# Kernel optimization log

Hardware: AMD Instinct MI355X
Metric: run time of the kernel (lower is better)

The kernel has to match this reference:

```python
import jax, jax.numpy as jnp
import numpy as np

B, DIM, T = 8, 1024, 2048      # batch, hidden_size, frames
CD, K, Q = 128, 1024, 8        # codebook_dim, codebook_size, num_quantizers


def setup_inputs() -> dict:
    key = jax.random.key(0)
    ks = jax.random.split(key, 5)
    return {
        "embeddings": jax.random.normal(ks[0], (B, DIM, T), jnp.float32),
        # stacked per-quantizer params (scan axis = Q)
        "W_in": jax.random.normal(ks[1], (Q, DIM, CD), jnp.float32) * 0.02,
        "b_in": jnp.zeros((Q, CD), jnp.float32),
        "W_out": jax.random.normal(ks[2], (Q, CD, DIM), jnp.float32) * 0.02,
        "b_out": jnp.zeros((Q, DIM), jnp.float32),
        "embed": jax.random.normal(ks[3], (Q, K, CD), jnp.float32),
    }


def _rvq_forward(embeddings, W_in, b_in, W_out, b_out, embed):
    """Residual VQ: sequentially quantize residual with Q euclidean codebooks.
    Returns (quantized_sum [B,DIM,T], codes [Q,B,T])."""

    def step(carry, params):
        residual, acc = carry
        Wi, bi, Wo, bo, E = params
        # project_in after permute(0,2,1): [B,T,CD]
        h = jnp.einsum('bdt,dc->btc', residual, Wi) + bi
        # squared euclidean distance to codebook entries: [B,T,K]
        dist = (h * h).sum(-1)[..., None] - 2.0 * jnp.einsum('btc,kc->btk', h, E) + (E * E).sum(-1)
        idx = jnp.argmin(dist, axis=-1)  # [B,T]
        # decode: gather codebook entry, project_out, permute back to [B,DIM,T]
        q = jnp.einsum('btc,cd->bdt', E[idx], Wo) + bo[:, None]
        return (residual - q, acc + q), idx

    init = (embeddings, jnp.zeros_like(embeddings))
    (_, quantized), codes = jax.lax.scan(step, init, (W_in, b_in, W_out, b_out, embed))
    return quantized, codes


def reference(embeddings, W_in, b_in, W_out, b_out, embed):
    quantized, _codes = _rvq_forward(embeddings, W_in, b_in, W_out, b_out, embed)
    return quantized
```

## Files before the change

### kernel.cpp

```cpp
#include <hip/hip_runtime.h>
#include <hip/hip_bf16.h>
#include <math.h>

#define BB   8
#define DIMM 1024
#define TT   2048
#define CDD  128
#define KK   1024
#define QQ   8
#define MM   (BB*TT)
#define NPAIR 28

typedef __attribute__((ext_vector_type(8))) short bf16x8;
typedef __attribute__((ext_vector_type(4))) float f32x4;

static __device__ __forceinline__ unsigned short f2bf(float f) {
    __hip_bfloat16 h = __float2bfloat16(f);
    unsigned short u; __builtin_memcpy(&u, &h, 2); return u;
}
static __device__ __forceinline__ float bf2f(unsigned short u) {
    __hip_bfloat16 h; __builtin_memcpy(&h, &u, 2); return __bfloat162float(h);
}

__global__ __launch_bounds__(256) void prep_embT(
    const float* __restrict__ emb,
    unsigned short* __restrict__ Th, unsigned short* __restrict__ Tm,
    unsigned short* __restrict__ Tl)
{
    __shared__ float tile[32][36];
    const int t0 = blockIdx.x * 32, d0 = blockIdx.y * 32, b = blockIdx.z;
    const int tid = threadIdx.x;
    {
        int r = tid >> 3, cg = (tid & 7) << 2;
        *(float4*)&tile[r][cg] =
            *(const float4*)(emb + ((size_t)b * DIMM + d0 + r) * TT + t0 + cg);
    }
    __syncthreads();
    {
        int tt = tid >> 3, dg = (tid & 7) << 2;
        unsigned short h4[4], m4[4], l4[4];
        #pragma unroll
        for (int u = 0; u < 4; u++) {
            float v = tile[dg + u][tt];
            h4[u] = f2bf(v);              float v1 = bf2f(h4[u]);
            m4[u] = f2bf(v - v1);         float v2 = bf2f(m4[u]);
            l4[u] = f2bf(v - v1 - v2);
        }
        size_t o = ((size_t)b * TT + t0 + tt) * DIMM + d0 + dg;
        *(ushort4*)(Th + o) = *(ushort4*)h4;
        *(ushort4*)(Tm + o) = *(ushort4*)m4;
        *(ushort4*)(Tl + o) = *(ushort4*)l4;
    }
}

__global__ __launch_bounds__(256) void prep_wiT(
    const float* __restrict__ Wi,
    unsigned short* __restrict__ Th, unsigned short* __restrict__ Tm,
    unsigned short* __restrict__ Tl)
{
    __shared__ float tile[32][36];
    const int d0 = blockIdx.x * 32, c0 = blockIdx.y * 32, q = blockIdx.z;
    const int tid = threadIdx.x;
    {
        int r = tid >> 3, cg = (tid & 7) << 2;
        *(float4*)&tile[r][cg] =
            *(const float4*)(Wi + ((size_t)q * DIMM + d0 + r) * CDD + c0 + cg);
    }
    __syncthreads();
    {
        int cc = tid >> 3, dg = (tid & 7) << 2;
        unsigned short h4[4], m4[4], l4[4];
        #pragma unroll
        for (int u = 0; u < 4; u++) {
            float v = tile[dg + u][cc];
            h4[u] = f2bf(v);              float v1 = bf2f(h4[u]);
            m4[u] = f2bf(v - v1);         float v2 = bf2f(m4[u]);
            l4[u] = f2bf(v - v1 - v2);
        }
        size_t o = ((size_t)q * CDD + c0 + cc) * DIMM + d0 + dg;
        *(ushort4*)(Th + o) = *(ushort4*)h4;
        *(ushort4*)(Tm + o) = *(ushort4*)m4;
        *(ushort4*)(Tl + o) = *(ushort4*)l4;
    }
}

__global__ __launch_bounds__(256) void prep_woT(
    const float* __restrict__ Wo,
    unsigned short* __restrict__ Th, unsigned short* __restrict__ Tl)
{
    __shared__ float tile[32][36];
    const int c0 = blockIdx.x * 32, d0 = blockIdx.y * 32, q = blockIdx.z;
    const int tid = threadIdx.x;
    {
        int r = tid >> 3, dg = (tid & 7) << 2;
        *(float4*)&tile[r][dg] =
            *(const float4*)(Wo + ((size_t)q * CDD + c0 + r) * DIMM + d0 + dg);
    }
    __syncthreads();
    {
        int dd = tid >> 3, cg = (tid & 7) << 2;
        unsigned short h4[4], l4[4];
        #pragma unroll
        for (int u = 0; u < 4; u++) {
            float v = tile[cg + u][dd];
            h4[u] = f2bf(v);
            l4[u] = f2bf(v - bf2f(h4[u]));
        }
        size_t o = ((size_t)q * DIMM + d0 + dd) * CDD + c0 + cg;
        *(ushort4*)(Th + o) = *(ushort4*)h4;
        *(ushort4*)(Tl + o) = *(ushort4*)l4;
    }
}

__global__ __launch_bounds__(64) void prep_esplit(
    const float* __restrict__ E,
    unsigned short* __restrict__ Eh, unsigned short* __restrict__ El,
    float* __restrict__ en)
{
    int row = blockIdx.x, lane = threadIdx.x;
    const float* e = E + (size_t)row * CDD;
    float v0 = e[lane * 2], v1 = e[lane * 2 + 1];
    unsigned short h2[2], l2[2];
    h2[0] = f2bf(v0); l2[0] = f2bf(v0 - bf2f(h2[0]));
    h2[1] = f2bf(v1); l2[1] = f2bf(v1 - bf2f(h2[1]));
    size_t o = (size_t)row * CDD + lane * 2;
    *(ushort2*)(Eh + o) = *(ushort2*)h2;
    *(ushort2*)(El + o) = *(ushort2*)l2;
    float s = v0 * v0 + v1 * v1;
    #pragma unroll
    for (int off = 32; off > 0; off >>= 1) s += __shfl_down(s, off);
    if (lane == 0) en[row] = s;
}

__global__ __launch_bounds__(256) void prep_pb(const float* __restrict__ bo,
                                               float* __restrict__ Pb)
{
    int d = blockIdx.x * 256 + threadIdx.x;
    float s = 0.f;
    Pb[d] = 0.f;
    for (int q = 0; q < QQ; q++) {
        s += bo[(size_t)q * DIMM + d];
        Pb[(size_t)(q + 1) * DIMM + d] = s;
    }
}

__global__ __launch_bounds__(128) void prep_cvec(const float* __restrict__ Pb,
                                                 const float* __restrict__ Wi,
                                                 float* __restrict__ cvec)
{
    int q = blockIdx.x, c = threadIdx.x;
    float s = 0.f;
    for (int d = 0; d < DIMM; d++)
        s = fmaf(Pb[(size_t)q * DIMM + d], Wi[((size_t)q * DIMM + d) * CDD + c], s);
    cvec[(size_t)q * CDD + c] = s;
}

__global__ __launch_bounds__(256) void k_hemb6(
    const unsigned short* __restrict__ A0, const unsigned short* __restrict__ A1,
    const unsigned short* __restrict__ A2,
    const unsigned short* __restrict__ B0g, const unsigned short* __restrict__ B1g,
    const unsigned short* __restrict__ B2g,
    const float* __restrict__ biAll, float* __restrict__ hembAll)
{
    const int q = blockIdx.z;
    const unsigned short* Bq0 = B0g + (size_t)q * CDD * DIMM;
    const unsigned short* Bq1 = B1g + (size_t)q * CDD * DIMM;
    const unsigned short* Bq2 = B2g + (size_t)q * CDD * DIMM;
    const float* bias = biAll + (size_t)q * CDD;
    float* C = hembAll + (size_t)q * MM * CDD;

    __shared__ unsigned short sA[3][128 * 40];
    __shared__ unsigned short sB[3][128 * 40];
    const int tid = threadIdx.x, lane = tid & 63, w = tid >> 6;
    const int wy = w >> 1, wx = w & 1;
    const int col = lane & 15, quad = lane >> 4;
    const int m0 = blockIdx.x * 128;

    f32x4 acc[4][4];
    #pragma unroll
    for (int i = 0; i < 4; i++)
        #pragma unroll
        for (int j = 0; j < 4; j++) acc[i][j] = (f32x4){0.f, 0.f, 0.f, 0.f};

    const int r = tid >> 1, s = (tid & 1) << 4;
    const int so = r * 40 + s;

    for (int k0 = 0; k0 < DIMM; k0 += 32) {
        {
            size_t ga = (size_t)(m0 + r) * DIMM + k0 + s;
            size_t gb = (size_t)r * DIMM + k0 + s;
            *(bf16x8*)(sA[0] + so)     = *(const bf16x8*)(A0 + ga);
            *(bf16x8*)(sA[0] + so + 8) = *(const bf16x8*)(A0 + ga + 8);
            *(bf16x8*)(sA[1] + so)     = *(const bf16x8*)(A1 + ga);
            *(bf16x8*)(sA[1] + so + 8) = *(const bf16x8*)(A1 + ga + 8);
            *(bf16x8*)(sA[2] + so)     = *(const bf16x8*)(A2 + ga);
            *(bf16x8*)(sA[2] + so + 8) = *(const bf16x8*)(A2 + ga + 8);
            *(bf16x8*)(sB[0] + so)     = *(const bf16x8*)(Bq0 + gb);
            *(bf16x8*)(sB[0] + so + 8) = *(const bf16x8*)(Bq0 + gb + 8);
            *(bf16x8*)(sB[1] + so)     = *(const bf16x8*)(Bq1 + gb);
            *(bf16x8*)(sB[1] + so + 8) = *(const bf16x8*)(Bq1 + gb + 8);
            *(bf16x8*)(sB[2] + so)     = *(const bf16x8*)(Bq2 + gb);
            *(bf16x8*)(sB[2] + so + 8) = *(const bf16x8*)(Bq2 + gb + 8);
        }
        __syncthreads();

        bf16x8 b0[4], b1[4], b2[4];
        #pragma unroll
        for (int nt = 0; nt < 4; nt++) {
            int rr = wx * 64 + nt * 16 + col;
            int o = rr * 40 + quad * 8;
            b0[nt] = *(const bf16x8*)(sB[0] + o);
            b1[nt] = *(const bf16x8*)(sB[1] + o);
            b2[nt] = *(const bf16x8*)(sB[2] + o);
        }
        #pragma unroll
        for (int mt = 0; mt < 4; mt++) {
            int rr = wy * 64 + mt * 16 + col;
            int o = rr * 40 + quad * 8;
            bf16x8 a0 = *(const bf16x8*)(sA[0] + o);
            bf16x8 a1 = *(const bf16x8*)(sA[1] + o);
            bf16x8 a2 = *(const bf16x8*)(sA[2] + o);
            #pragma unroll
            for (int nt = 0; nt < 4; nt++) {
                f32x4 a = acc[mt][nt];
                a = __builtin_amdgcn_mfma_f32_16x16x32_bf16(a0, b0[nt], a, 0, 0, 0);
                a = __builtin_amdgcn_mfma_f32_16x16x32_bf16(a1, b0[nt], a, 0, 0, 0);
                a = __builtin_amdgcn_mfma_f32_16x16x32_bf16(a2, b0[nt], a, 0, 0, 0);
                a = __builtin_amdgcn_mfma_f32_16x16x32_bf16(a0, b1[nt], a, 0, 0, 0);
                a = __builtin_amdgcn_mfma_f32_16x16x32_bf16(a1, b1[nt], a, 0, 0, 0);
                a = __builtin_amdgcn_mfma_f32_16x16x32_bf16(a0, b2[nt], a, 0, 0, 0);
                acc[mt][nt] = a;
            }
        }
        __syncthreads();
    }
    #pragma unroll
    for (int nt = 0; nt < 4; nt++) {
        int n = wx * 64 + nt * 16 + col;
        float bv = bias[n];
        #pragma unroll
        for (int mt = 0; mt < 4; mt++) {
            #pragma unroll
            for (int rr = 0; rr < 4; rr++) {
                int m = m0 + wy * 64 + mt * 16 + quad * 4 + rr;
                C[(size_t)m * CDD + n] = acc[mt][nt][rr] + bv;
            }
        }
    }
}

__device__ __forceinline__ void gemm3p_core(
    const unsigned short* __restrict__ Ah, const unsigned short* __restrict__ Al,
    const unsigned short* __restrict__ Bh, const unsigned short* __restrict__ Bl,
    float* __restrict__ C, int ldc, const float* __restrict__ bias,
    int K, int m0, int n0)
{
    __shared__ unsigned short sAh[128 * 72], sAl[128 * 72];
    __shared__ unsigned short sBh[128 * 72], sBl[128 * 72];
    const int tid = threadIdx.x, lane = tid & 63, w = tid >> 6;
    const int wy = w >> 1, wx = w & 1;
    const int col = lane & 15, quad = lane >> 4;

    f32x4 acc[4][4];
    #pragma unroll
    for (int i = 0; i < 4; i++)
        #pragma unroll
        for (int j = 0; j < 4; j++) acc[i][j] = (f32x4){0.f, 0.f, 0.f, 0.f};

    for (int k0 = 0; k0 < K; k0 += 64) {
        int r = tid >> 1, s = (tid & 1) * 32;
        {
            const unsigned short* ga = Ah + (size_t)(m0 + r) * K + k0 + s;
            const unsigned short* gl = Al + (size_t)(m0 + r) * K + k0 + s;
            const unsigned short* gb = Bh + (size_t)(n0 + r) * K + k0 + s;
            const unsigned short* gc = Bl + (size_t)(n0 + r) * K + k0 + s;
            int o = r * 72 + s;
            #pragma unroll
            for (int u = 0; u < 4; u++) {
                *(bf16x8*)(sAh + o + u * 8) = *(const bf16x8*)(ga + u * 8);
                *(bf16x8*)(sAl + o + u * 8) = *(const bf16x8*)(gl + u * 8);
                *(bf16x8*)(sBh + o + u * 8) = *(const bf16x8*)(gb + u * 8);
                *(bf16x8*)(sBl + o + u * 8) = *(const bf16x8*)(gc + u * 8);
            }
        }
        __syncthreads();
        #pragma unroll
        for (int ks = 0; ks < 2; ks++) {
            bf16x8 ah[4], al[4], bh[4], bl[4];
            int oo = ((ks << 2) + quad) << 3;
            #pragma unroll
            for (int mt = 0; mt < 4; mt++) {
                int rr = wy * 64 + mt * 16 + col;
                ah[mt] = *(const bf16x8*)(sAh + rr * 72 + oo);
                al[mt] = *(const bf16x8*)(sAl + rr * 72 + oo);
            }
            #pragma unroll
            for (int nt = 0; nt < 4; nt++) {
                int rr = wx * 64 + nt * 16 + col;
                bh[nt] = *(const bf16x8*)(sBh + rr * 72 + oo);
                bl[nt] = *(const bf16x8*)(sBl + rr * 72 + oo);
            }
            #pragma unroll
            for (int mt = 0; mt < 4; mt++)
                #pragma unroll
                for (int nt = 0; nt < 4; nt++) {
                    f32x4 a = acc[mt][nt];
                    a = __builtin_amdgcn_mfma_f32_16x16x32_bf16(ah[mt], bh[nt], a, 0, 0, 0);
                    a = __builtin_amdgcn_mfma_f32_16x16x32_bf16(al[mt], bh[nt], a, 0, 0, 0);
                    a = __builtin_amdgcn_mfma_f32_16x16x32_bf16(ah[mt], bl[nt], a, 0, 0, 0);
                    acc[mt][nt] = a;
                }
        }
        __syncthreads();
    }
    #pragma unroll
    for (int nt = 0; nt < 4; nt++) {
        int n = n0 + wx * 64 + nt * 16 + col;
        float bv = bias ? bias[n - n0] : 0.f;
        #pragma unroll
        for (int mt = 0; mt < 4; mt++) {
            #pragma unroll
            for (int rr = 0; rr < 4; rr++) {
                int m = m0 + wy * 64 + mt * 16 + quad * 4 + rr;
                C[(size_t)m * ldc + n] = acc[mt][nt][rr] + bv;
            }
        }
    }
}

__global__ __launch_bounds__(256) void k_D(
    const unsigned short* __restrict__ Eh, const unsigned short* __restrict__ El,
    const unsigned short* __restrict__ WoTh, const unsigned short* __restrict__ WoTl,
    float* __restrict__ D)
{
    int p = blockIdx.z;
    gemm3p_core(Eh + (size_t)p * KK * CDD, El + (size_t)p * KK * CDD,
                WoTh + (size_t)p * DIMM * CDD, WoTl + (size_t)p * DIMM * CDD,
                D + (size_t)p * KK * DIMM, DIMM, nullptr,
                CDD, blockIdx.x * 128, blockIdx.y * 128);
}

__device__ __forceinline__ void f32gemm64(
    const float* __restrict__ A, int lda, const float* __restrict__ B, int ldb,
    float* __restrict__ C, int ldc, int K, int m0, int n0)
{
    __shared__ float As[32][68];
    __shared__ float Bs[32][68];
    const int tid = threadIdx.x, tx = tid & 15, ty = tid >> 4;
    float dot[4][4];
    #pragma unroll
    for (int i = 0; i < 4; i++)
        #pragma unroll
        for (int j = 0; j < 4; j++) dot[i][j] = 0.f;

    for (int k0 = 0; k0 < K; k0 += 32) {
        #pragma unroll
        for (int i = 0; i < 2; i++) {
            int j = i * 256 + tid;
            int r = j >> 3, kc = (j & 7) << 2;
            float4 a = *(const float4*)(A + (size_t)(m0 + r) * lda + k0 + kc);
            As[kc + 0][r] = a.x; As[kc + 1][r] = a.y;
            As[kc + 2][r] = a.z; As[kc + 3][r] = a.w;
        }
        #pragma unroll
        for (int i = 0; i < 2; i++) {
            int j = i * 256 + tid;
            int kr = j >> 4, nc = (j & 15) << 2;
            *(float4*)&Bs[kr][nc] = *(const float4*)(B + (size_t)(k0 + kr) * ldb + n0 + nc);
        }
        __syncthreads();
        #pragma unroll 4
        for (int kk = 0; kk < 32; kk++) {
            float4 a4 = *(float4*)&As[kk][ty << 2];
            float4 b4 = *(float4*)&Bs[kk][tx << 2];
            float av[4] = {a4.x, a4.y, a4.z, a4.w};
            float bv[4] = {b4.x, b4.y, b4.z, b4.w};
            #pragma unroll
            for (int i = 0; i < 4; i++)
                #pragma unroll
                for (int j = 0; j < 4; j++)
                    dot[i][j] = fmaf(av[i], bv[j], dot[i][j]);
        }
        __syncthreads();
    }
    #pragma unroll
    for (int i = 0; i < 4; i++)
        *(float4*)(C + (size_t)(m0 + (ty << 2) + i) * ldc + n0 + (tx << 2)) =
            *(float4*)&dot[i][0];
}

__global__ __launch_bounds__(256) void gemm_G(
    const float* __restrict__ Wo, const float* __restrict__ Wi, float* __restrict__ G)
{
    int z = blockIdx.z, p = z, q = 1;
    while (p >= q) { p -= q; q++; }
    f32gemm64(Wo + (size_t)p * CDD * DIMM, DIMM,
              Wi + (size_t)q * DIMM * CDD, CDD,
              G + (size_t)z * CDD * CDD, CDD, DIMM,
              blockIdx.y * 64, blockIdx.x * 64);
}

__global__ __launch_bounds__(256) void gemm_F(
    const float* __restrict__ E, const float* __restrict__ G, float* __restrict__ F)
{
    int z = blockIdx.z, p = z, q = 1;
    while (p >= q) { p -= q; q++; }
    f32gemm64(E + (size_t)p * KK * CDD, CDD,
              G + (size_t)z * CDD * CDD, CDD,
              F + (size_t)z * KK * CDD, CDD, CDD,
              blockIdx.y * 64, blockIdx.x * 64);
}

__device__ __forceinline__ void top4_insert(float (&v)[4], int (&id)[4],
                                            float nv, int nid) {
    if (nv < v[3] || (nv == v[3] && nid < id[3])) {
        v[3] = nv; id[3] = nid;
        #pragma unroll
        for (int p = 3; p > 0; p--) {
            if (v[p] < v[p - 1] || (v[p] == v[p - 1] && id[p] < id[p - 1])) {
                float tv = v[p]; v[p] = v[p - 1]; v[p - 1] = tv;
                int ti = id[p]; id[p] = id[p - 1]; id[p - 1] = ti;
            } else break;
        }
    }
}

__global__ __launch_bounds__(256) void chain_pa(
    const float* __restrict__ hemb_q, const float* __restrict__ Fq,
    const float* __restrict__ cvec_q, const int* __restrict__ idx_all, int q,
    const unsigned short* __restrict__ EhT_q, const unsigned short* __restrict__ ElT_q,
    const float* __restrict__ Ef_q, const float* __restrict__ en_q,
    int* __restrict__ idx_out)
{
    __shared__ __align__(16) char smem[51712];
    float* Hs = (float*)smem;
    unsigned short* Esh = (unsigned short*)(smem + 16896);
    unsigned short* Esl = Esh + 64 * 136;
    float* candv = (float*)(smem + 16896);
    int*   candi = (int*)(smem + 16896 + 16384);

    const int tid = threadIdx.x;
    const int m0 = blockIdx.x * 32;
    const int lane = tid & 63, w = tid >> 6;
    const int col = lane & 15, quad = lane >> 4;

    {
        int t = tid >> 3, cg = (tid & 7) << 4;
        float hv[16];
        const float* hp = hemb_q + (size_t)(m0 + t) * CDD + cg;
        #pragma unroll
        for (int u = 0; u < 4; u++) *(float4*)&hv[u * 4] = *(const float4*)(hp + u * 4);
        const float* cv = cvec_q + cg;
        #pragma unroll
        for (int u = 0; u < 16; u++) hv[u] -= cv[u];
        for (int p = 0; p < q; p++) {
            int k = idx_all[(size_t)p * MM + m0 + t];
            const float* fp = Fq + ((size_t)p * KK + k) * CDD + cg;
            #pragma unroll
            for (int u = 0; u < 4; u++) {
                float4 f4 = *(const float4*)(fp + u * 4);
                hv[u * 4 + 0] -= f4.x; hv[u * 4 + 1] -= f4.y;
                hv[u * 4 + 2] -= f4.z; hv[u * 4 + 3] -= f4.w;
            }
        }
        float* hd = Hs + t * 132 + cg;
        #pragma unroll
        for (int u = 0; u < 4; u++) *(float4*)(hd + u * 4) = *(float4*)&hv[u * 4];
    }
    __syncthreads();

    bf16x8 ah[2][4], al[2][4];
    #pragma unroll
    for (int m = 0; m < 2; m++) {
        int t = m * 16 + col;
        #pragma unroll
        for (int ks = 0; ks < 4; ks++) {
            const float* hp = Hs + t * 132 + ks * 32 + quad * 8;
            float v[8];
            *(f32x4*)(v) = *(const f32x4*)(hp);
            *(f32x4*)(v + 4) = *(const f32x4*)(hp + 4);
            short hs[8], ls[8];
            #pragma unroll
            for (int u = 0; u < 8; u++) {
                unsigned short u1 = f2bf(v[u]);
                hs[u] = (short)u1;
                ls[u] = (short)f2bf(v[u] - bf2f(u1));
            }
            ah[m][ks] = (bf16x8){hs[0],hs[1],hs[2],hs[3],hs[4],hs[5],hs[6],hs[7]};
            al[m][ks] = (bf16x8){ls[0],ls[1],ls[2],ls[3],ls[4],ls[5],ls[6],ls[7]};
        }
    }

    float tv1[8], tv2[8]; int ti1[8], ti2[8];
    #pragma unroll
    for (int s = 0; s < 8; s++) { tv1[s] = INFINITY; tv2[s] = INFINITY;
                                  ti1[s] = 1 << 30; ti2[s] = 1 << 30; }
    const int lc = (w << 4) + col;

    for (int k0 = 0; k0 < KK; k0 += 64) {
        {
            int row = tid >> 2, seg = (tid & 3) << 5;
            const unsigned short* gh = EhT_q + (size_t)(k0 + row) * CDD + seg;
            const unsigned short* gl = ElT_q + (size_t)(k0 + row) * CDD + seg;
            int o = row * 136 + seg;
            *(bf16x8*)(Esh + o)     = *(const bf16x8*)(gh);
            *(bf16x8*)(Esh + o + 8) = *(const bf16x8*)(gh + 8);
            *(bf16x8*)(Esh + o +16) = *(const bf16x8*)(gh + 16);
            *(bf16x8*)(Esh + o +24) = *(const bf16x8*)(gh + 24);
            *(bf16x8*)(Esl + o)     = *(const bf16x8*)(gl);
            *(bf16x8*)(Esl + o + 8) = *(const bf16x8*)(gl + 8);
            *(bf16x8*)(Esl + o +16) = *(const bf16x8*)(gl + 16);
            *(bf16x8*)(Esl + o +24) = *(const bf16x8*)(gl + 24);
        }
        __syncthreads();

        bf16x8 bh[4], bl[4];
        #pragma unroll
        for (int ks = 0; ks < 4; ks++) {
            int o = lc * 136 + (((ks << 2) + quad) << 3);
            bh[ks] = *(const bf16x8*)(Esh + o);
            bl[ks] = *(const bf16x8*)(Esl + o);
        }
        f32x4 d2[2];
        #pragma unroll
        for (int m = 0; m < 2; m++) {
            f32x4 dd = (f32x4){0.f, 0.f, 0.f, 0.f};
            #pragma unroll
            for (int ks = 0; ks < 4; ks++) {
                dd = __builtin_amdgcn_mfma_f32_16x16x32_bf16(ah[m][ks], bh[ks], dd, 0, 0, 0);
                dd = __builtin_amdgcn_mfma_f32_16x16x32_bf16(al[m][ks], bh[ks], dd, 0, 0, 0);
                dd = __builtin_amdgcn_mfma_f32_16x16x32_bf16(ah[m][ks], bl[ks], dd, 0, 0, 0);
            }
            d2[m] = dd;
        }
        int kcode = k0 + lc;
        float env = en_q[kcode];
        #pragma unroll
        for (int m = 0; m < 2; m++)
            #pragma unroll
            for (int rr = 0; rr < 4; rr++) {
                float dist = fmaf(-2.f, d2[m][rr], env);
                int s = (m << 2) + rr;
                if (dist < tv1[s]) { tv2[s] = tv1[s]; ti2[s] = ti1[s];
                                     tv1[s] = dist;   ti1[s] = kcode; }
                else if (dist < tv2[s]) { tv2[s] = dist; ti2[s] = kcode; }
            }
        __syncthreads();
    }

    #pragma unroll
    for (int m = 0; m < 2; m++)
        #pragma unroll
        for (int rr = 0; rr < 4; rr++) {
            int t = m * 16 + (quad << 2) + rr;
            int s = (m << 2) + rr;
            int base = t * 128 + lc * 2;
            candv[base] = tv1[s];     candi[base] = ti1[s];
            candv[base + 1] = tv2[s]; candi[base + 1] = ti2[s];
        }
    __syncthreads();

    {
        int t = tid >> 3, j = tid & 7;
        float v[4]; int id[4];
        #pragma unroll
        for (int p = 0; p < 4; p++) { v[p] = INFINITY; id[p] = 1 << 30; }
        #pragma unroll
        for (int e = 0; e < 16; e++)
            top4_insert(v, id, candv[t * 128 + j * 16 + e], candi[t * 128 + j * 16 + e]);
        #pragma unroll
        for (int d = 1; d < 8; d <<= 1) {
            #pragma unroll
            for (int s = 0; s < 4; s++) {
                float pv = __shfl_xor(v[s], d);
                int   pi = __shfl_xor(id[s], d);
                top4_insert(v, id, pv, pi);
            }
        }
        int cand = id[j & 3];
        const float* er = Ef_q + (size_t)cand * CDD + ((j >> 2) << 6);
        const float* hr = Hs + t * 132 + ((j >> 2) << 6);
        float dot = 0.f;
        #pragma unroll 8
        for (int c = 0; c < 64; c++) dot = fmaf(hr[c], er[c], dot);
        dot += __shfl_xor(dot, 4);
        float dist = fmaf(-2.f, dot, en_q[cand]);
        #pragma unroll
        for (int d = 1; d < 4; d <<= 1) {
            float ov = __shfl_xor(dist, d);
            int   oi = __shfl_xor(cand, d);
            if (ov < dist || (ov == dist && oi < cand)) { dist = ov; cand = oi; }
        }
        if (j == 0) idx_out[m0 + t] = cand;
    }
}

__global__ __launch_bounds__(256) void final_out(
    const int* __restrict__ idx_all, const float* __restrict__ D,
    const float* __restrict__ PbFull, float* __restrict__ out)
{
    __shared__ int ids[QQ][64];
    const int tid = threadIdx.x;
    const int m0 = blockIdx.x * 64, d0 = blockIdx.y * 64;
    const int b = m0 / TT, t0 = m0 % TT;
    const int tx = tid & 15, ty = tid >> 4;
    #pragma unroll
    for (int e = 0; e < 2; e++) {
        int j = e * 256 + tid;
        int p = j >> 6, tt = j & 63;
        ids[p][tt] = idx_all[(size_t)p * MM + m0 + tt];
    }
    __syncthreads();

    float s[4][4];
    #pragma unroll
    for (int j = 0; j < 4; j++) {
        float bs = PbFull[d0 + (ty << 2) + j];
        #pragma unroll
        for (int i = 0; i < 4; i++) s[i][j] = bs;
    }
    #pragma unroll
    for (int p = 0; p < QQ; p++) {
        #pragma unroll
        for (int i = 0; i < 4; i++) {
            int row = ids[p][tx + (i << 4)];
            float4 dv = *(const float4*)(D + ((size_t)p * KK + row) * DIMM + d0 + (ty << 2));
            s[i][0] += dv.x; s[i][1] += dv.y; s[i][2] += dv.z; s[i][3] += dv.w;
        }
    }
    #pragma unroll
    for (int j = 0; j < 4; j++) {
        float* base = out + (size_t)b * DIMM * TT + (size_t)(d0 + (ty << 2) + j) * TT + t0 + tx;
        #pragma unroll
        for (int i = 0; i < 4; i++) base[i << 4] = s[i][j];
    }
}

extern "C" void kernel_launch(void* const* d_in, const int* in_sizes, int n_in,
                              void* d_out, int out_size, void* d_ws, size_t ws_size,
                              hipStream_t stream) {
    const float* emb   = (const float*)d_in[0];
    const float* W_in  = (const float*)d_in[1];
    const float* b_in  = (const float*)d_in[2];
    const float* W_out = (const float*)d_in[3];
    const float* b_out = (const float*)d_in[4];
    const float* embed = (const float*)d_in[5];
    float* out = (float*)d_out;

    char* ws = (char*)d_ws;
    size_t off = 0;
    auto alloc = [&](size_t bytes) { char* p = ws + off; off = (off + bytes + 255) & ~(size_t)255; return p; };
    int*   idxbuf = (int*)alloc((size_t)QQ * MM * 4);
    float* en     = (float*)alloc((size_t)QQ * KK * 4);
    unsigned short* EhT = (unsigned short*)alloc((size_t)QQ * KK * CDD * 2);
    unsigned short* ElT = (unsigned short*)alloc((size_t)QQ * KK * CDD * 2);
    unsigned short* WiTh = (unsigned short*)alloc((size_t)QQ * CDD * DIMM * 2);
    unsigned short* WiTm = (unsigned short*)alloc((size_t)QQ * CDD * DIMM * 2);
    unsigned short* WiTl = (unsigned short*)alloc((size_t)QQ * CDD * DIMM * 2);
    unsigned short* WoTh = (unsigned short*)alloc((size_t)QQ * DIMM * CDD * 2);
    unsigned short* WoTl = (unsigned short*)alloc((size_t)QQ * DIMM * CDD * 2);
    unsigned short* embTh = (unsigned short*)alloc((size_t)MM * DIMM * 2);
    unsigned short* embTm = (unsigned short*)alloc((size_t)MM * DIMM * 2);
    unsigned short* embTl = (unsigned short*)alloc((size_t)MM * DIMM * 2);
    float* hemb = (float*)alloc((size_t)QQ * MM * CDD * 4);
    float* G    = (float*)alloc((size_t)NPAIR * CDD * CDD * 4);
    float* F    = (float*)alloc((size_t)NPAIR * KK * CDD * 4);
    float* D    = (float*)alloc((size_t)QQ * KK * DIMM * 4);
    float* Pb   = (float*)alloc((size_t)(QQ + 1) * DIMM * 4);
    float* cvec = (float*)alloc((size_t)QQ * CDD * 4);

    prep_embT<<<dim3(TT / 32, DIMM / 32, BB), 256, 0, stream>>>(emb, embTh, embTm, embTl);
    prep_wiT<<<dim3(DIMM / 32, CDD / 32, QQ), 256, 0, stream>>>(W_in, WiTh, WiTm, WiTl);
    prep_woT<<<dim3(CDD / 32, DIMM / 32, QQ), 256, 0, stream>>>(W_out, WoTh, WoTl);
    prep_esplit<<<QQ * KK, 64, 0, stream>>>(embed, EhT, ElT, en);
    prep_pb<<<DIMM / 256, 256, 0, stream>>>(b_out, Pb);
    prep_cvec<<<QQ, 128, 0, stream>>>(Pb, W_in, cvec);

    k_hemb6<<<dim3(MM / 128, 1, QQ), 256, 0, stream>>>(
        embTh, embTm, embTl, WiTh, WiTm, WiTl, b_in, hemb);
    gemm_G<<<dim3(2, 2, NPAIR), 256, 0, stream>>>(W_out, W_in, G);
    gemm_F<<<dim3(2, 16, NPAIR), 256, 0, stream>>>(embed, G, F);
    k_D<<<dim3(KK / 128, DIMM / 128, QQ), 256, 0, stream>>>(EhT, ElT, WoTh, WoTl, D);

    for (int q = 0; q < QQ; q++) {
        chain_pa<<<MM / 32, 256, 0, stream>>>(
            hemb + (size_t)q * MM * CDD,
            F + (size_t)(q * (q - 1) / 2) * KK * CDD,
            cvec + (size_t)q * CDD,
            idxbuf, q,
            EhT + (size_t)q * KK * CDD, ElT + (size_t)q * KK * CDD,
            embed + (size_t)q * KK * CDD, en + (size_t)q * KK,
            idxbuf + (size_t)q * MM);
    }
    final_out<<<dim3(MM / 64, DIMM / 64), 256, 0, stream>>>(idxbuf, D, Pb + (size_t)QQ * DIMM, out);
}
```

Before: 926.6 us.

## Load B operands directly from global memory instead of staging through LDS

```diff
diff --git a/kernel.cpp b/kernel.cpp
--- a/kernel.cpp
+++ b/kernel.cpp
@@ -170,7 +170,6 @@
     float* C = hembAll + (size_t)q * MM * CDD;
 
     __shared__ unsigned short sA[3][128 * 40];
-    __shared__ unsigned short sB[3][128 * 40];
     const int tid = threadIdx.x, lane = tid & 63, w = tid >> 6;
     const int wy = w >> 1, wx = w & 1;
     const int col = lane & 15, quad = lane >> 4;
@@ -182,36 +181,32 @@
         #pragma unroll
         for (int j = 0; j < 4; j++) acc[i][j] = (f32x4){0.f, 0.f, 0.f, 0.f};
 
-    const int r = tid >> 1, s = (tid & 1) << 4;
+    const int r = tid & 127, s = (tid >> 7) << 4;
     const int so = r * 40 + s;
+
+    size_t boff[4];
+    #pragma unroll
+    for (int nt = 0; nt < 4; nt++)
+        boff[nt] = (size_t)(wx * 64 + nt * 16 + col) * DIMM + quad * 8;
 
     for (int k0 = 0; k0 < DIMM; k0 += 32) {
         {
             size_t ga = (size_t)(m0 + r) * DIMM + k0 + s;
-            size_t gb = (size_t)r * DIMM + k0 + s;
             *(bf16x8*)(sA[0] + so)     = *(const bf16x8*)(A0 + ga);
             *(bf16x8*)(sA[0] + so + 8) = *(const bf16x8*)(A0 + ga + 8);
             *(bf16x8*)(sA[1] + so)     = *(const bf16x8*)(A1 + ga);
             *(bf16x8*)(sA[1] + so + 8) = *(const bf16x8*)(A1 + ga + 8);
             *(bf16x8*)(sA[2] + so)     = *(const bf16x8*)(A2 + ga);
             *(bf16x8*)(sA[2] + so + 8) = *(const bf16x8*)(A2 + ga + 8);
-            *(bf16x8*)(sB[0] + so)     = *(const bf16x8*)(Bq0 + gb);
-            *(bf16x8*)(sB[0] + so + 8) = *(const bf16x8*)(Bq0 + gb + 8);
-            *(bf16x8*)(sB[1] + so)     = *(const bf16x8*)(Bq1 + gb);
-            *(bf16x8*)(sB[1] + so + 8) = *(const bf16x8*)(Bq1 + gb + 8);
-            *(bf16x8*)(sB[2] + so)     = *(const bf16x8*)(Bq2 + gb);
-            *(bf16x8*)(sB[2] + so + 8) = *(const bf16x8*)(Bq2 + gb + 8);
         }
         __syncthreads();
 
         bf16x8 b0[4], b1[4], b2[4];
         #pragma unroll
         for (int nt = 0; nt < 4; nt++) {
-            int rr = wx * 64 + nt * 16 + col;
-            int o = rr * 40 + quad * 8;
-            b0[nt] = *(const bf16x8*)(sB[0] + o);
-            b1[nt] = *(const bf16x8*)(sB[1] + o);
-            b2[nt] = *(const bf16x8*)(sB[2] + o);
+            b0[nt] = *(const bf16x8*)(Bq0 + boff[nt] + k0);
+            b1[nt] = *(const bf16x8*)(Bq1 + boff[nt] + k0);
+            b2[nt] = *(const bf16x8*)(Bq2 + boff[nt] + k0);
         }
         #pragma unroll
         for (int mt = 0; mt < 4; mt++) {
@@ -432,10 +427,8 @@
     const float* __restrict__ Ef_q, const float* __restrict__ en_q,
     int* __restrict__ idx_out)
 {
-    __shared__ __align__(16) char smem[51712];
-    float* Hs = (float*)smem;
-    unsigned short* Esh = (unsigned short*)(smem + 16896);
-    unsigned short* Esl = Esh + 64 * 136;
+    __shared__ __align__(16) char smem[49664];
+    float* Hs    = (float*)smem;
     float* candv = (float*)(smem + 16896);
     int*   candi = (int*)(smem + 16896 + 16384);
 
@@ -498,28 +491,14 @@
     const int lc = (w << 4) + col;
 
     for (int k0 = 0; k0 < KK; k0 += 64) {
-        {
-            int row = tid >> 2, seg = (tid & 3) << 5;
-            const unsigned short* gh = EhT_q + (size_t)(k0 + row) * CDD + seg;
-            const unsigned short* gl = ElT_q + (size_t)(k0 + row) * CDD + seg;
-            int o = row * 136 + seg;
-            *(bf16x8*)(Esh + o)     = *(const bf16x8*)(gh);
-            *(bf16x8*)(Esh + o + 8) = *(const bf16x8*)(gh + 8);
-            *(bf16x8*)(Esh + o +16) = *(const bf16x8*)(gh + 16);
-            *(bf16x8*)(Esh + o +24) = *(const bf16x8*)(gh + 24);
-            *(bf16x8*)(Esl + o)     = *(const bf16x8*)(gl);
-            *(bf16x8*)(Esl + o + 8) = *(const bf16x8*)(gl + 8);
-            *(bf16x8*)(Esl + o +16) = *(const bf16x8*)(gl + 16);
-            *(bf16x8*)(Esl + o +24) = *(const bf16x8*)(gl + 24);
-        }
-        __syncthreads();
-
         bf16x8 bh[4], bl[4];
+        const unsigned short* gh = EhT_q + (size_t)(k0 + lc) * CDD;
+        const unsigned short* gl = ElT_q + (size_t)(k0 + lc) * CDD;
         #pragma unroll
         for (int ks = 0; ks < 4; ks++) {
-            int o = lc * 136 + (((ks << 2) + quad) << 3);
-            bh[ks] = *(const bf16x8*)(Esh + o);
-            bl[ks] = *(const bf16x8*)(Esl + o);
+            int o = (((ks << 2) + quad) << 3);
+            bh[ks] = *(const bf16x8*)(gh + o);
+            bl[ks] = *(const bf16x8*)(gl + o);
         }
         f32x4 d2[2];
         #pragma unroll
@@ -545,7 +524,6 @@
                                      tv1[s] = dist;   ti1[s] = kcode; }
                 else if (dist < tv2[s]) { tv2[s] = dist; ti2[s] = kcode; }
             }
-        __syncthreads();
     }
 
     #pragma unroll
```

New measurement: 990.8 us. 1.07x slower.
